# Kernel optimization log

Measured on AMD Instinct MI355X. Metric: run time of the kernel, lower is better.

## Reference

```python
import jax, jax.numpy as jnp
import numpy as np

NUM_NODES = 100000
NUM_EDGES = 1600000
NUM_GRAPHS = 512
F_IN = 128
HID = 128
N_CLASSES = 10
N_HIDDEN_LAYERS = 3


def _gcn_layer(x, W, b, src, dst, dinv, num_nodes):
    # PyG GCNConv: h = X W; out_i = sum_j norm_ij * h_j; out += bias
    h = x @ W                                  # [N, H]
    norm = dinv[src] * dinv[dst]               # [E'] edge norms (incl. self-loops)
    msg = h[src] * norm[:, None]               # [E', H] gather + scale
    out = jax.ops.segment_sum(msg, dst, num_segments=num_nodes)  # scatter-add
    return out + b


def setup_inputs() -> dict:
    key = jax.random.key(0)
    ks = jax.random.split(key, 12)
    x = jax.random.normal(ks[0], (NUM_NODES, F_IN), dtype=jnp.float32)
    edge_index = jax.random.randint(ks[1], (2, NUM_EDGES), 0, NUM_NODES, dtype=jnp.int64)
    batch = jnp.sort(jax.random.randint(ks[2], (NUM_NODES,), 0, NUM_GRAPHS, dtype=jnp.int64))
    s = 1.0 / np.sqrt(HID)
    W0 = jax.random.uniform(ks[3], (F_IN, HID), jnp.float32, -s, s)
    b0 = jnp.zeros((HID,), jnp.float32)
    W1 = jax.random.uniform(ks[4], (HID, HID), jnp.float32, -s, s)
    b1 = jnp.zeros((HID,), jnp.float32)
    W2 = jax.random.uniform(ks[5], (HID, HID), jnp.float32, -s, s)
    b2 = jnp.zeros((HID,), jnp.float32)
    W3 = jax.random.uniform(ks[6], (HID, HID), jnp.float32, -s, s)
    b3 = jnp.zeros((HID,), jnp.float32)
    Wl = jax.random.uniform(ks[7], (HID, N_CLASSES), jnp.float32, -s, s)
    bl = jnp.zeros((N_CLASSES,), jnp.float32)
    return {"x": x, "edge_index": edge_index, "batch": batch,
            "W0": W0, "b0": b0, "W1": W1, "b1": b1, "W2": W2, "b2": b2,
            "W3": W3, "b3": b3, "Wl": Wl, "bl": bl}


def reference(x, edge_index, batch, W0, b0, W1, b1, W2, b2, W3, b3, Wl, bl):
    n = x.shape[0]
    loops = jnp.arange(n, dtype=edge_index.dtype)
    src = jnp.concatenate([edge_index[0], loops])   # add self-loops
    dst = jnp.concatenate([edge_index[1], loops])
    deg = jax.ops.segment_sum(jnp.ones(dst.shape[0], x.dtype), dst, num_segments=n)
    dinv = jnp.where(deg > 0, jax.lax.rsqrt(deg), 0.0)

    h = jax.nn.relu(_gcn_layer(x, W0, b0, src, dst, dinv, n))
    for W, b in ((W1, b1), (W2, b2), (W3, b3)):
        h = jax.nn.relu(_gcn_layer(h, W, b, src, dst, dinv, n))

    # global_mean_pool over graph ids
    counts = jax.ops.segment_sum(jnp.ones(n, h.dtype), batch, num_segments=NUM_GRAPHS)
    pooled = jax.ops.segment_sum(h, batch, num_segments=NUM_GRAPHS)
    global_mean = pooled / jnp.maximum(counts, 1.0)[:, None]

    # dropout is identity in eval mode
    y = global_mean @ Wl + bl
    return (y, global_mean)
```

## Files before the change

### kernel.cpp

```cpp
#include <hip/hip_runtime.h>


#define ATOMIC_ADD_F32(p, v) __hip_atomic_fetch_add((p), (v), __ATOMIC_RELAXED, __HIP_MEMORY_SCOPE_AGENT)

constexpr int NG = 512;
constexpr float LO_SCALE = 4096.f;
constexpr float LO_INV   = 1.f / 4096.f;

typedef _Float16 half8 __attribute__((ext_vector_type(8)));
typedef _Float16 half4 __attribute__((ext_vector_type(4)));
typedef float f32x4 __attribute__((ext_vector_type(4)));

__global__ __launch_bounds__(256) void k_deg_init(int* __restrict__ deg, int N) {
    int i = blockIdx.x * 256 + threadIdx.x;
    if (i < N) deg[i] = 1;
}

__global__ __launch_bounds__(256) void k_deg_count_xcd(const int* __restrict__ dst,
                                                       int* __restrict__ deg,
                                                       int E, int N) {
    const int range = blockIdx.x & 7;
    const int chunk = blockIdx.x >> 3;
    const int nchunks = gridDim.x >> 3;
    const int csz = (E + nchunks - 1) / nchunks;
    const int lo = chunk * csz;
    const int hi = min(lo + csz, E);
    const int nr = N / 8;
    const int rlo = range * nr;
    const int rhi = (range == 7) ? N : rlo + nr;
    for (int i = lo + threadIdx.x; i < hi; i += 256) {
        int d = dst[i];
        if (d >= rlo && d < rhi) atomicAdd(&deg[d], 1);
    }
}

__global__ __launch_bounds__(256) void k_scan_local(const int* __restrict__ deg,
                                                    int* __restrict__ rowptr,
                                                    int* __restrict__ partials,
                                                    float* __restrict__ dinv, int N) {
    __shared__ int s[256];
    int t = threadIdx.x;
    int i = blockIdx.x * 256 + t;
    int dg = (i < N) ? deg[i] : 1;
    if (i < N) dinv[i] = rsqrtf((float)dg);
    int v = (i < N) ? (dg - 1) : 0;
    s[t] = v;
    __syncthreads();
#pragma unroll
    for (int off = 1; off < 256; off <<= 1) {
        int add = (t >= off) ? s[t - off] : 0;
        __syncthreads();
        s[t] += add;
        __syncthreads();
    }
    if (i < N) rowptr[i] = s[t] - v;
    if (t == 255) partials[blockIdx.x] = s[t];
}

__global__ __launch_bounds__(512) void k_scan_partials(int* __restrict__ partials, int nblk) {
    __shared__ int s[512];
    int t = threadIdx.x;
    int v = (t < nblk) ? partials[t] : 0;
    s[t] = v;
    __syncthreads();
#pragma unroll
    for (int off = 1; off < 512; off <<= 1) {
        int add = (t >= off) ? s[t - off] : 0;
        __syncthreads();
        s[t] += add;
        __syncthreads();
    }
    if (t < nblk) partials[t] = s[t] - v;
}

__global__ __launch_bounds__(256) void k_scan_apply(const int* __restrict__ deg,
                                                    int* __restrict__ rowptr,
                                                    int* __restrict__ cursor,
                                                    const int* __restrict__ partials, int N) {
    int i = blockIdx.x * 256 + threadIdx.x;
    if (i < N) {
        int r = rowptr[i] + partials[blockIdx.x];
        rowptr[i] = r;
        cursor[i] = r;
        if (i == N - 1) rowptr[N] = r + deg[i] - 1;
    }
}

__global__ __launch_bounds__(256) void k_csr_fill_xcd(const int* __restrict__ src,
                                                      const int* __restrict__ dst,
                                                      int* __restrict__ cursor,
                                                      int* __restrict__ csr_src,
                                                      int E, int N) {
    const int range = blockIdx.x & 7;
    const int chunk = blockIdx.x >> 3;
    const int nchunks = gridDim.x >> 3;
    const int csz = (E + nchunks - 1) / nchunks;
    const int lo = chunk * csz;
    const int hi = min(lo + csz, E);
    const int nr = N / 8;
    const int rlo = range * nr;
    const int rhi = (range == 7) ? N : rlo + nr;
    for (int i = lo + threadIdx.x; i < hi; i += 256) {
        int d = dst[i];
        if (d >= rlo && d < rhi) {
            int pos = atomicAdd(&cursor[d], 1);
            csr_src[pos] = src[i];
        }
    }
}

struct WSplitArgs {
    const float* W[4];
    _Float16* Wth[4];
    _Float16* Wtl[4];
};
__global__ __launch_bounds__(256) void k_wsplit4(WSplitArgs a) {
    int idx = blockIdx.x * 256 + threadIdx.x;
    int layer = idx >> 14;
    int e = idx & 16383;
    int k = e >> 7, c = e & 127;
    float w = a.W[layer][e];
    _Float16 hi = (_Float16)w;
    float lo = (w - (float)hi) * LO_SCALE;
    a.Wth[layer][c * 128 + k] = hi;
    a.Wtl[layer][c * 128 + k] = (_Float16)lo;
}

__global__ __launch_bounds__(256) void k_xhalf(const float* __restrict__ X,
                                               _Float16* __restrict__ Xh, int total) {
    int i = (blockIdx.x * 256 + threadIdx.x) * 4;
    if (i < total) {
        float4 v = *(const float4*)(X + i);
        half4 h = { (_Float16)v.x, (_Float16)v.y, (_Float16)v.z, (_Float16)v.w };
        *(half4*)(Xh + i) = h;
    }
}

__global__ __launch_bounds__(256) void k_gemm_f16(const _Float16* __restrict__ A,
                                                  const _Float16* __restrict__ Wth,
                                                  const _Float16* __restrict__ Wtl,
                                                  const float* __restrict__ dinv,
                                                  _Float16* __restrict__ Hh, int N) {
    const int tid = threadIdx.x;
    const int wave = tid >> 6;
    const int l = tid & 63;
    const int wrow = wave & 1;
    const int wcol = wave >> 1;
    const int lr = l & 15;
    const int lkb = (l >> 4) * 8;

    const int row_base = blockIdx.x * 64 + wrow * 32;
    const int c_base = wcol * 64;

    f32x4 acch[2][4], accl[2][4];
#pragma unroll
    for (int rt = 0; rt < 2; ++rt)
#pragma unroll
        for (int ct = 0; ct < 4; ++ct) {
            acch[rt][ct] = (f32x4){0.f, 0.f, 0.f, 0.f};
            accl[rt][ct] = (f32x4){0.f, 0.f, 0.f, 0.f};
        }

#pragma unroll
    for (int ks = 0; ks < 4; ++ks) {
        const int koff = ks * 32 + lkb;

        half8 bh[4], bl[4];
#pragma unroll
        for (int ct = 0; ct < 4; ++ct) {
            size_t off = (size_t)(c_base + ct * 16 + lr) * 128 + koff;
            bh[ct] = *(const half8*)(Wth + off);
            bl[ct] = *(const half8*)(Wtl + off);
        }

        half8 a[2];
#pragma unroll
        for (int rt = 0; rt < 2; ++rt) {
            int r = row_base + rt * 16 + lr;
            if (r >= N) r = N - 1;
            a[rt] = *(const half8*)(A + (size_t)r * 128 + koff);
        }

#pragma unroll
        for (int rt = 0; rt < 2; ++rt)
#pragma unroll
            for (int ct = 0; ct < 4; ++ct) {
                acch[rt][ct] = __builtin_amdgcn_mfma_f32_16x16x32_f16(a[rt], bh[ct], acch[rt][ct], 0, 0, 0);
                accl[rt][ct] = __builtin_amdgcn_mfma_f32_16x16x32_f16(a[rt], bl[ct], accl[rt][ct], 0, 0, 0);
            }
    }

#pragma unroll
    for (int rt = 0; rt < 2; ++rt) {
        int r0 = row_base + rt * 16 + (l >> 4) * 4;
        float dv[4];
#pragma unroll
        for (int j = 0; j < 4; ++j) dv[j] = (r0 + j < N) ? dinv[r0 + j] : 0.f;
#pragma unroll
        for (int ct = 0; ct < 4; ++ct) {
            int col = c_base + ct * 16 + lr;
#pragma unroll
            for (int j = 0; j < 4; ++j) {
                int r = r0 + j;
                if (r < N) {
                    float v = fmaf(accl[rt][ct][j], LO_INV, acch[rt][ct][j]);
                    Hh[(size_t)r * 128 + col] = (_Float16)(v * dv[j]);
                }
            }
        }
    }
}

__global__ __launch_bounds__(256) void k_aggregate_f16(const int* __restrict__ csr_src,
                                                       const int* __restrict__ rowptr,
                                                       const float* __restrict__ dinv,
                                                       const _Float16* __restrict__ Hh,
                                                       const float* __restrict__ bias,
                                                       _Float16* __restrict__ Ah, int N) {
    int d = blockIdx.x * 4 + (threadIdx.x >> 6);
    if (d >= N) return;
    const int lane = threadIdx.x & 63;
    const unsigned* Hu = (const unsigned*)Hh;

    int beg = rowptr[d], end = rowptr[d + 1];
    union PK { unsigned u; _Float16 h[2]; };

    PK sv; sv.u = Hu[(size_t)d * 64 + lane];
    float ax = (float)sv.h[0];
    float ay = (float)sv.h[1];

    int j = beg;
    for (; j + 7 < end; j += 8) {
        int s[8]; PK v[8];
#pragma unroll
        for (int u = 0; u < 8; ++u) s[u] = csr_src[j + u];
#pragma unroll
        for (int u = 0; u < 8; ++u) v[u].u = Hu[(size_t)s[u] * 64 + lane];
#pragma unroll
        for (int u = 0; u < 8; ++u) {
            ax += (float)v[u].h[0];
            ay += (float)v[u].h[1];
        }
    }
    for (; j < end; ++j) {
        PK v; v.u = Hu[(size_t)csr_src[j] * 64 + lane];
        ax += (float)v.h[0];
        ay += (float)v.h[1];
    }

    float dd = dinv[d];
    float2 b2 = ((const float2*)bias)[lane];
    ax = fmaxf(fmaf(dd, ax, b2.x), 0.f);
    ay = fmaxf(fmaf(dd, ay, b2.y), 0.f);

    PK o; o.h[0] = (_Float16)ax; o.h[1] = (_Float16)ay;
    ((unsigned*)Ah)[(size_t)d * 64 + lane] = o.u;
}

__global__ __launch_bounds__(128) void k_pool(const _Float16* __restrict__ A,
                                              const int* __restrict__ batch,
                                              float* __restrict__ pooled,
                                              float* __restrict__ counts, int N) {
    int k = threadIdx.x;
    int i0 = blockIdx.x * 64;
    if (i0 >= N) return;
    int iend = min(i0 + 64, N);
    float acc = 0.f;
    int cnt = 0;
    int cur = batch[i0];
    for (int i = i0; i < iend; ++i) {
        int g = batch[i];
        if (g != cur) {
            ATOMIC_ADD_F32(&pooled[cur * 128 + k], acc);
            if (k == 0) ATOMIC_ADD_F32(&counts[cur], (float)cnt);
            acc = 0.f; cnt = 0; cur = g;
        }
        acc += (float)A[(size_t)i * 128 + k];
        cnt++;
    }
    ATOMIC_ADD_F32(&pooled[cur * 128 + k], acc);
    if (k == 0) ATOMIC_ADD_F32(&counts[cur], (float)cnt);
}

__global__ __launch_bounds__(128) void k_finalize(const float* __restrict__ pooled,
                                                  const float* __restrict__ counts,
                                                  const float* __restrict__ Wl,
                                                  const float* __restrict__ bl,
                                                  float* __restrict__ out) {
    int g = blockIdx.x;
    int t = threadIdx.x;
    __shared__ float m[128];
    float c = fmaxf(counts[g], 1.f);
    float mean = pooled[g * 128 + t] / c;
    out[NG * 10 + g * 128 + t] = mean;
    m[t] = mean;
    __syncthreads();
    if (t < 10) {
        float acc = bl[t];
#pragma unroll 16
        for (int k = 0; k < 128; ++k) acc = fmaf(m[k], Wl[k * 10 + t], acc);
        out[g * 10 + t] = acc;
    }
}

extern "C" void kernel_launch(void* const* d_in, const int* in_sizes, int n_in,
                              void* d_out, int out_size, void* d_ws, size_t ws_size,
                              hipStream_t stream) {
    const float* x     = (const float*)d_in[0];
    const int*   ei    = (const int*)d_in[1];
    const int*   batch = (const int*)d_in[2];
    const float* Wt[4] = { (const float*)d_in[3], (const float*)d_in[5],
                           (const float*)d_in[7], (const float*)d_in[9] };
    const float* bt[4] = { (const float*)d_in[4], (const float*)d_in[6],
                           (const float*)d_in[8], (const float*)d_in[10] };
    const float* Wl = (const float*)d_in[11];
    const float* bl = (const float*)d_in[12];
    float* out = (float*)d_out;

    const int N = in_sizes[0] / 128;
    const int E = in_sizes[1] / 2;
    const int* src = ei;
    const int* dst = ei + E;

    char* p = (char*)d_ws;
    _Float16* Xh    = (_Float16*)p;  p += (size_t)N * 128 * 2;
    _Float16* Hh    = (_Float16*)p;  p += (size_t)N * 128 * 2;
    _Float16* Ah    = (_Float16*)p;  p += (size_t)N * 128 * 2;
    float* dinv     = (float*)p;     p += (size_t)N * 4;
    int*   deg      = (int*)p;       p += (size_t)N * 4;
    int*   rowptr   = (int*)p;       p += (size_t)(N + 1) * 4;
    int*   cursor   = (int*)p;       p += (size_t)N * 4;
    int*   csr_src  = (int*)p;       p += (size_t)E * 4;
    int*   partials = (int*)p;       p += 512 * 4;
    float* pooled   = (float*)p;     p += (size_t)NG * 128 * 4;
    float* counts   = (float*)p;     p += (size_t)NG * 4;
    _Float16* Wsp   = (_Float16*)p;  p += 4 * 2 * 128 * 128 * 2;

    const int nblk = (N + 255) / 256;

    k_deg_init<<<nblk, 256, 0, stream>>>(deg, N);
    k_deg_count_xcd<<<2048, 256, 0, stream>>>(dst, deg, E, N);

    k_scan_local<<<nblk, 256, 0, stream>>>(deg, rowptr, partials, dinv, N);
    k_scan_partials<<<1, 512, 0, stream>>>(partials, nblk);
    k_scan_apply<<<nblk, 256, 0, stream>>>(deg, rowptr, cursor, partials, N);
    k_csr_fill_xcd<<<2048, 256, 0, stream>>>(src, dst, cursor, csr_src, E, N);

    WSplitArgs wa;
    _Float16* Wth[4]; _Float16* Wtl[4];
    for (int l = 0; l < 4; ++l) {
        Wth[l] = Wsp + (size_t)l * 2 * 16384;
        Wtl[l] = Wth[l] + 16384;
        wa.W[l] = Wt[l];
        wa.Wth[l] = Wth[l];
        wa.Wtl[l] = Wtl[l];
    }
    k_wsplit4<<<256, 256, 0, stream>>>(wa);
    k_xhalf<<<(N * 128 / 4 + 255) / 256, 256, 0, stream>>>(x, Xh, N * 128);

    const int gemm_blocks = (N + 63) / 64;
    const int agg_blocks = (N + 3) / 4;
    const _Float16* in = Xh;
    for (int l = 0; l < 4; ++l) {
        k_gemm_f16<<<gemm_blocks, 256, 0, stream>>>(in, Wth[l], Wtl[l], dinv, Hh, N);
        k_aggregate_f16<<<agg_blocks, 256, 0, stream>>>(csr_src, rowptr, dinv, Hh, bt[l], Ah, N);
        in = Ah;
    }

    hipMemsetAsync(pooled, 0, (size_t)(NG * 128 + NG) * 4, stream);
    k_pool<<<(N + 63) / 64, 128, 0, stream>>>(Ah, batch, pooled, counts, N);
    k_finalize<<<NG, 128, 0, stream>>>(pooled, counts, Wl, bl, out);
}
```

Measured before the change: 678.7 us.

## Reorder GCN layer to aggregate-then-transform and fuse into one kernel

Uses (A X) W = A (X W) to aggregate the pre-scaled input features first and then multiply by W inside a single per-layer kernel. The aggregated 64-row tile is staged in shared memory and fed to the MFMA GEMM, with bias, ReLU and the next layer's dinv pre-scaling applied in the epilogue. This removes the intermediate H buffer write/read and one kernel launch per layer, and folds the dinv scaling of the input into the fp16 conversion. The cost is that each block serializes gather then GEMM with no overlap between the two, and fewer, heavier blocks may lower occupancy. Degree init also moves to a memset.

```diff
diff --git a/kernel.cpp b/kernel.cpp
--- a/kernel.cpp
+++ b/kernel.cpp
@@ -10,11 +10,6 @@
 typedef _Float16 half8 __attribute__((ext_vector_type(8)));
 typedef _Float16 half4 __attribute__((ext_vector_type(4)));
 typedef float f32x4 __attribute__((ext_vector_type(4)));
-
-__global__ __launch_bounds__(256) void k_deg_init(int* __restrict__ deg, int N) {
-    int i = blockIdx.x * 256 + threadIdx.x;
-    if (i < N) deg[i] = 1;
-}
 
 __global__ __launch_bounds__(256) void k_deg_count_xcd(const int* __restrict__ dst,
                                                        int* __restrict__ deg,
@@ -41,10 +36,9 @@
     __shared__ int s[256];
     int t = threadIdx.x;
     int i = blockIdx.x * 256 + t;
-    int dg = (i < N) ? deg[i] : 1;
-    if (i < N) dinv[i] = rsqrtf((float)dg);
-    int v = (i < N) ? (dg - 1) : 0;
-    s[t] = v;
+    int dg = (i < N) ? deg[i] : 0;
+    if (i < N) dinv[i] = rsqrtf((float)(dg + 1));
+    s[t] = dg;
     __syncthreads();
 #pragma unroll
     for (int off = 1; off < 256; off <<= 1) {
@@ -53,7 +47,7 @@
         s[t] += add;
         __syncthreads();
     }
-    if (i < N) rowptr[i] = s[t] - v;
+    if (i < N) rowptr[i] = s[t] - dg;
     if (t == 255) partials[blockIdx.x] = s[t];
 }
 
@@ -82,7 +76,7 @@
         int r = rowptr[i] + partials[blockIdx.x];
         rowptr[i] = r;
         cursor[i] = r;
-        if (i == N - 1) rowptr[N] = r + deg[i] - 1;
+        if (i == N - 1) rowptr[N] = r + deg[i];
     }
 }
 
@@ -126,30 +120,69 @@
     a.Wtl[layer][c * 128 + k] = (_Float16)lo;
 }
 
-__global__ __launch_bounds__(256) void k_xhalf(const float* __restrict__ X,
-                                               _Float16* __restrict__ Xh, int total) {
-    int i = (blockIdx.x * 256 + threadIdx.x) * 4;
-    if (i < total) {
-        float4 v = *(const float4*)(X + i);
-        half4 h = { (_Float16)v.x, (_Float16)v.y, (_Float16)v.z, (_Float16)v.w };
-        *(half4*)(Xh + i) = h;
-    }
-}
-
-__global__ __launch_bounds__(256) void k_gemm_f16(const _Float16* __restrict__ A,
-                                                  const _Float16* __restrict__ Wth,
-                                                  const _Float16* __restrict__ Wtl,
-                                                  const float* __restrict__ dinv,
-                                                  _Float16* __restrict__ Hh, int N) {
+__global__ __launch_bounds__(256) void k_xscale(const float* __restrict__ X,
+                                                const float* __restrict__ dinv,
+                                                _Float16* __restrict__ P, int N) {
+    int i = blockIdx.x * 256 + threadIdx.x;
+    if (i >= N * 32) return;
+    float dd = dinv[i >> 5];
+    float4 v = ((const float4*)X)[i];
+    half4 h = { (_Float16)(v.x * dd), (_Float16)(v.y * dd),
+                (_Float16)(v.z * dd), (_Float16)(v.w * dd) };
+    ((half4*)P)[i] = h;
+}
+
+__global__ __launch_bounds__(256) void k_layer(const int* __restrict__ csr_src,
+                                               const int* __restrict__ rowptr,
+                                               const float* __restrict__ dinv,
+                                               const _Float16* __restrict__ P,
+                                               const _Float16* __restrict__ Wth,
+                                               const _Float16* __restrict__ Wtl,
+                                               const float* __restrict__ bias,
+                                               _Float16* __restrict__ Pout,
+                                               int N, int last) {
+    __shared__ char Ms[64 * 272];
     const int tid = threadIdx.x;
     const int wave = tid >> 6;
-    const int l = tid & 63;
+    const int lane = tid & 63;
+    const int row0 = blockIdx.x * 64;
+    const unsigned* Pu = (const unsigned*)P;
+
+    union PK { unsigned u; _Float16 h[2]; };
+
+    for (int r = wave * 16; r < wave * 16 + 16; ++r) {
+        int d = row0 + r;
+        float ax = 0.f, ay = 0.f;
+        if (d < N) {
+            PK v; v.u = Pu[(size_t)d * 64 + lane];
+            ax = (float)v.h[0]; ay = (float)v.h[1];
+            int beg = rowptr[d], end = rowptr[d + 1];
+            int j = beg;
+            for (; j + 7 < end; j += 8) {
+                int s[8]; PK t[8];
+#pragma unroll
+                for (int u = 0; u < 8; ++u) s[u] = csr_src[j + u];
+#pragma unroll
+                for (int u = 0; u < 8; ++u) t[u].u = Pu[(size_t)s[u] * 64 + lane];
+#pragma unroll
+                for (int u = 0; u < 8; ++u) { ax += (float)t[u].h[0]; ay += (float)t[u].h[1]; }
+            }
+            for (; j < end; ++j) {
+                PK t; t.u = Pu[(size_t)csr_src[j] * 64 + lane];
+                ax += (float)t.h[0]; ay += (float)t.h[1];
+            }
+            float dd = dinv[d];
+            ax *= dd; ay *= dd;
+        }
+        PK o; o.h[0] = (_Float16)ax; o.h[1] = (_Float16)ay;
+        *(unsigned*)(Ms + r * 272 + lane * 4) = o.u;
+    }
+    __syncthreads();
+
     const int wrow = wave & 1;
     const int wcol = wave >> 1;
-    const int lr = l & 15;
-    const int lkb = (l >> 4) * 8;
-
-    const int row_base = blockIdx.x * 64 + wrow * 32;
+    const int lr = lane & 15;
+    const int q = lane >> 4;
     const int c_base = wcol * 64;
 
     f32x4 acch[2][4], accl[2][4];
@@ -163,24 +196,19 @@
 
 #pragma unroll
     for (int ks = 0; ks < 4; ++ks) {
-        const int koff = ks * 32 + lkb;
-
         half8 bh[4], bl[4];
 #pragma unroll
         for (int ct = 0; ct < 4; ++ct) {
-            size_t off = (size_t)(c_base + ct * 16 + lr) * 128 + koff;
+            size_t off = (size_t)(c_base + ct * 16 + lr) * 128 + ks * 32 + q * 8;
             bh[ct] = *(const half8*)(Wth + off);
             bl[ct] = *(const half8*)(Wtl + off);
         }
-
         half8 a[2];
 #pragma unroll
         for (int rt = 0; rt < 2; ++rt) {
-            int r = row_base + rt * 16 + lr;
-            if (r >= N) r = N - 1;
-            a[rt] = *(const half8*)(A + (size_t)r * 128 + koff);
-        }
-
+            int lrow = wrow * 32 + rt * 16 + lr;
+            a[rt] = *(const half8*)(Ms + lrow * 272 + ks * 64 + q * 16);
+        }
 #pragma unroll
         for (int rt = 0; rt < 2; ++rt)
 #pragma unroll
@@ -190,12 +218,19 @@
             }
     }
 
+    float bcol[4];
+#pragma unroll
+    for (int ct = 0; ct < 4; ++ct) bcol[ct] = bias[c_base + ct * 16 + lr];
+
 #pragma unroll
     for (int rt = 0; rt < 2; ++rt) {
-        int r0 = row_base + rt * 16 + (l >> 4) * 4;
+        int r0 = row0 + wrow * 32 + rt * 16 + q * 4;
         float dv[4];
 #pragma unroll
-        for (int j = 0; j < 4; ++j) dv[j] = (r0 + j < N) ? dinv[r0 + j] : 0.f;
+        for (int j = 0; j < 4; ++j) {
+            int r = r0 + j;
+            dv[j] = (!last && r < N) ? dinv[r] : 1.f;
+        }
 #pragma unroll
         for (int ct = 0; ct < 4; ++ct) {
             int col = c_base + ct * 16 + lr;
@@ -203,58 +238,13 @@
             for (int j = 0; j < 4; ++j) {
                 int r = r0 + j;
                 if (r < N) {
-                    float v = fmaf(accl[rt][ct][j], LO_INV, acch[rt][ct][j]);
-                    Hh[(size_t)r * 128 + col] = (_Float16)(v * dv[j]);
+                    float v = fmaf(accl[rt][ct][j], LO_INV, acch[rt][ct][j]) + bcol[ct];
+                    v = fmaxf(v, 0.f);
+                    Pout[(size_t)r * 128 + col] = (_Float16)(v * dv[j]);
                 }
             }
         }
     }
-}
-
-__global__ __launch_bounds__(256) void k_aggregate_f16(const int* __restrict__ csr_src,
-                                                       const int* __restrict__ rowptr,
-                                                       const float* __restrict__ dinv,
-                                                       const _Float16* __restrict__ Hh,
-                                                       const float* __restrict__ bias,
-                                                       _Float16* __restrict__ Ah, int N) {
-    int d = blockIdx.x * 4 + (threadIdx.x >> 6);
-    if (d >= N) return;
-    const int lane = threadIdx.x & 63;
-    const unsigned* Hu = (const unsigned*)Hh;
-
-    int beg = rowptr[d], end = rowptr[d + 1];
-    union PK { unsigned u; _Float16 h[2]; };
-
-    PK sv; sv.u = Hu[(size_t)d * 64 + lane];
-    float ax = (float)sv.h[0];
-    float ay = (float)sv.h[1];
-
-    int j = beg;
-    for (; j + 7 < end; j += 8) {
-        int s[8]; PK v[8];
-#pragma unroll
-        for (int u = 0; u < 8; ++u) s[u] = csr_src[j + u];
-#pragma unroll
-        for (int u = 0; u < 8; ++u) v[u].u = Hu[(size_t)s[u] * 64 + lane];
-#pragma unroll
-        for (int u = 0; u < 8; ++u) {
-            ax += (float)v[u].h[0];
-            ay += (float)v[u].h[1];
-        }
-    }
-    for (; j < end; ++j) {
-        PK v; v.u = Hu[(size_t)csr_src[j] * 64 + lane];
-        ax += (float)v.h[0];
-        ay += (float)v.h[1];
-    }
-
-    float dd = dinv[d];
-    float2 b2 = ((const float2*)bias)[lane];
-    ax = fmaxf(fmaf(dd, ax, b2.x), 0.f);
-    ay = fmaxf(fmaf(dd, ay, b2.y), 0.f);
-
-    PK o; o.h[0] = (_Float16)ax; o.h[1] = (_Float16)ay;
-    ((unsigned*)Ah)[(size_t)d * 64 + lane] = o.u;
 }
 
 __global__ __launch_bounds__(128) void k_pool(const _Float16* __restrict__ A,
@@ -323,9 +313,8 @@
     const int* dst = ei + E;
 
     char* p = (char*)d_ws;
-    _Float16* Xh    = (_Float16*)p;  p += (size_t)N * 128 * 2;
-    _Float16* Hh    = (_Float16*)p;  p += (size_t)N * 128 * 2;
-    _Float16* Ah    = (_Float16*)p;  p += (size_t)N * 128 * 2;
+    _Float16* Pa    = (_Float16*)p;  p += (size_t)N * 128 * 2;
+    _Float16* Pb    = (_Float16*)p;  p += (size_t)N * 128 * 2;
     float* dinv     = (float*)p;     p += (size_t)N * 4;
     int*   deg      = (int*)p;       p += (size_t)N * 4;
     int*   rowptr   = (int*)p;       p += (size_t)(N + 1) * 4;
@@ -338,7 +327,7 @@
 
     const int nblk = (N + 255) / 256;
 
-    k_deg_init<<<nblk, 256, 0, stream>>>(deg, N);
+    hipMemsetAsync(deg, 0, (size_t)N * 4, stream);
     k_deg_count_xcd<<<2048, 256, 0, stream>>>(dst, deg, E, N);
 
     k_scan_local<<<nblk, 256, 0, stream>>>(deg, rowptr, partials, dinv, N);
@@ -356,18 +345,19 @@
         wa.Wtl[l] = Wtl[l];
     }
     k_wsplit4<<<256, 256, 0, stream>>>(wa);
-    k_xhalf<<<(N * 128 / 4 + 255) / 256, 256, 0, stream>>>(x, Xh, N * 128);
-
-    const int gemm_blocks = (N + 63) / 64;
-    const int agg_blocks = (N + 3) / 4;
-    const _Float16* in = Xh;
+    k_xscale<<<(N * 32 + 255) / 256, 256, 0, stream>>>(x, dinv, Pa, N);
+
+    const int layer_blocks = (N + 63) / 64;
+    _Float16* pin = Pa;
+    _Float16* pout = Pb;
     for (int l = 0; l < 4; ++l) {
-        k_gemm_f16<<<gemm_blocks, 256, 0, stream>>>(in, Wth[l], Wtl[l], dinv, Hh, N);
-        k_aggregate_f16<<<agg_blocks, 256, 0, stream>>>(csr_src, rowptr, dinv, Hh, bt[l], Ah, N);
-        in = Ah;
+        k_layer<<<layer_blocks, 256, 0, stream>>>(csr_src, rowptr, dinv, pin,
+                                                  Wth[l], Wtl[l], bt[l], pout,
+                                                  N, (l == 3) ? 1 : 0);
+        _Float16* tmp = pin; pin = pout; pout = tmp;
     }
 
     hipMemsetAsync(pooled, 0, (size_t)(NG * 128 + NG) * 4, stream);
-    k_pool<<<(N + 63) / 64, 128, 0, stream>>>(Ah, batch, pooled, counts, N);
+    k_pool<<<(N + 63) / 64, 128, 0, stream>>>(pin, batch, pooled, counts, N);
     k_finalize<<<NG, 128, 0, stream>>>(pooled, counts, Wl, bl, out);
 }
```

Measured after the change: 1.023 ms. 1.51x slower.
